# Optimization experiments

Measured on AMD Instinct MI355X. Metric: run time of the kernel, lower is better.

Reference implementation:

```python
import jax, jax.numpy as jnp
import numpy as np

N = 50000          # num nodes
E = 800000         # num edges
NUM_CLASSES = 40
FEAT_DIM = 256
FEAT_HID = 64
DEG_HID = 32
HID = 128
IN_CH = NUM_CLASSES + FEAT_HID + DEG_HID  # 136
MAX_DEG = 256      # degree-embedding table size (clip; random graph max deg << 256)


def _init_linear(key, fan_in, fan_out):
    kw, kb = jax.random.split(key)
    s = 1.0 / np.sqrt(fan_in)
    W = jax.random.uniform(kw, (fan_in, fan_out), jnp.float32, -s, s)
    b = jax.random.uniform(kb, (fan_out,), jnp.float32, -s, s)
    return W, b


def setup_inputs() -> dict:
    key = jax.random.key(0)
    ks = jax.random.split(key, 8)
    logits = jax.random.normal(ks[0], (N, NUM_CLASSES), jnp.float32)
    features = jax.random.normal(ks[1], (N, FEAT_DIM), jnp.float32)
    edge_index = jax.random.randint(ks[2], (2, E), 0, N, jnp.int32)
    Wf, bf = _init_linear(ks[3], FEAT_DIM, FEAT_HID)
    deg_table = jax.random.normal(ks[4], (MAX_DEG, DEG_HID), jnp.float32)
    W1, b1 = _init_linear(ks[5], IN_CH, HID)
    W2, b2 = _init_linear(ks[6], HID, HID)
    W3, b3 = _init_linear(ks[7], HID, NUM_CLASSES)
    return {"logits": logits, "features": features, "edge_index": edge_index,
            "Wf": Wf, "bf": bf, "deg_table": deg_table,
            "W1": W1, "b1": b1, "W2": W2, "b2": b2, "W3": W3, "b3": b3}


def reference(logits, features, edge_index, Wf, bf, deg_table, W1, b1, W2, b2, W3, b3):
    src, dst = edge_index[0], edge_index[1]
    # degree embedding: deg = degree(src) + degree(dst) on original edges
    ones_e = jnp.ones(src.shape[0], logits.dtype)
    deg = jax.ops.segment_sum(ones_e, src, num_segments=N) + \
          jax.ops.segment_sum(ones_e, dst, num_segments=N)
    deg_idx = jnp.clip(deg.astype(jnp.int32), 0, MAX_DEG - 1)
    deg_emb = deg_table[deg_idx]                              # [N, DEG_HID]

    x = jnp.concatenate([logits, features @ Wf + bf, deg_emb], axis=-1)  # [N, 136]

    # GCN normalization with self-loops (PyG gcn_norm): deg from dst column
    loop = jnp.arange(N, dtype=src.dtype)
    s = jnp.concatenate([src, loop])
    d = jnp.concatenate([dst, loop])
    dg = jax.ops.segment_sum(jnp.ones(d.shape[0], x.dtype), d, num_segments=N)
    dinv = jnp.where(dg > 0, jax.lax.rsqrt(dg), 0.0)
    norm = dinv[s] * dinv[d]                                  # [E+N]

    def conv(h, W, b):
        h = h @ W                                             # linear first
        msg = h[s] * norm[:, None]                            # gather + scale
        return jax.ops.segment_sum(msg, d, num_segments=N) + b

    x = jax.nn.relu(conv(x, W1, b1))   # dropout identity (inference)
    x = jax.nn.relu(conv(x, W2, b2))
    return conv(x, W3, b3)             # [N, NUM_CLASSES]
```

## Files before the change

kernel.cpp:

```cpp
#include <hip/hip_runtime.h>
#include <hip/hip_bf16.h>

constexpr int cN = 50000;
constexpr int cE = 800000;
constexpr int cNUM_CLASSES = 40;
constexpr int cFEAT_DIM = 256;
constexpr int cFEAT_HID = 64;
constexpr int cDEG_HID = 32;
constexpr int cHID = 128;
constexpr int cIN_CH = cNUM_CLASSES + cFEAT_HID + cDEG_HID;
constexpr int cKPAD = 160;
constexpr int cMAX_DEG = 256;
constexpr int cSCAN_NB = (cN + 255) / 256;

constexpr int cNCHUNK = 128;
constexpr int cCHUNK  = cE / cNCHUNK;
constexpr int cWORDS  = cN / 2;
constexpr int cHWORDS = cWORDS / 2;

typedef unsigned short ushort8_t __attribute__((ext_vector_type(8)));
typedef short short8_t __attribute__((ext_vector_type(8)));
typedef float float4_t __attribute__((ext_vector_type(4)));

__device__ __forceinline__ unsigned short f2bf(float f) {
    unsigned u = __builtin_bit_cast(unsigned, f);
    u += 0x7fff + ((u >> 16) & 1);
    return (unsigned short)(u >> 16);
}
__device__ __forceinline__ float bf2f(unsigned short s) {
    unsigned u = ((unsigned)s) << 16;
    return __builtin_bit_cast(float, u);
}

__global__ __launch_bounds__(256) void hist_kernel(const int* __restrict__ edge,
                                                   unsigned* __restrict__ partial) {
    __shared__ unsigned lds[cHWORDS];
    const int b = blockIdx.x, tid = threadIdx.x;
    const int cb = b & (cNCHUNK - 1);
    const int half = (b >> 7) & 1;
    const int which = b >> 8;
    for (int i = tid; i < cHWORDS; i += 256) lds[i] = 0;
    __syncthreads();
    const int* ids = edge + (size_t)which * cE + (size_t)cb * cCHUNK;
    const int lo = half * (cN / 2), hi = lo + cN / 2;
    const int wbase = half * cHWORDS;
    for (int i = tid; i < cCHUNK; i += 256) {
        int v = ids[i];
        if (v >= lo && v < hi)
            atomicAdd(&lds[(v >> 1) - wbase], 1u << ((v & 1) * 16));
    }
    __syncthreads();
    unsigned* outp = partial + ((size_t)which * cNCHUNK + cb) * cWORDS + wbase;
    for (int i = tid; i < cHWORDS; i += 256) outp[i] = lds[i];
}

__global__ __launch_bounds__(256) void merge_scan_kernel(unsigned* __restrict__ partial,
                                                         int* __restrict__ count_src,
                                                         int* __restrict__ count_dst) {
    const int w = blockIdx.x * 256 + threadIdx.x;
    if (w >= cWORDS) return;
    unsigned slo = 0, shi = 0;
    const unsigned* ps = partial + w;
    for (int c = 0; c < cNCHUNK; ++c) {
        unsigned v = ps[(size_t)c * cWORDS];
        slo += v & 0xFFFFu; shi += v >> 16;
    }
    *(int2*)&count_src[2 * w] = make_int2((int)slo, (int)shi);
    unsigned plo = 0, phi = 0;
    unsigned* pd = partial + (size_t)cNCHUNK * cWORDS + w;
    for (int c = 0; c < cNCHUNK; ++c) {
        unsigned v = pd[(size_t)c * cWORDS];
        pd[(size_t)c * cWORDS] = plo | (phi << 16);
        plo += v & 0xFFFFu; phi += v >> 16;
    }
    *(int2*)&count_dst[2 * w] = make_int2((int)plo, (int)phi);
}

__global__ __launch_bounds__(256) void block_sum_kernel(const int* __restrict__ cnt,
                                                        int* __restrict__ bsum) {
    __shared__ int s[256];
    int tid = threadIdx.x;
    int i = blockIdx.x * 256 + tid;
    int v = (i < cN) ? cnt[i] : 0;
    s[tid] = v;
    __syncthreads();
    #pragma unroll
    for (int off = 128; off > 0; off >>= 1) {
        if (tid < off) s[tid] += s[tid + off];
        __syncthreads();
    }
    if (tid == 0) bsum[blockIdx.x] = s[0];
}

__global__ __launch_bounds__(256) void scan_sums_kernel(const int* __restrict__ bsum,
                                                        int* __restrict__ boff) {
    __shared__ int s[256];
    int tid = threadIdx.x;
    int v = (tid < cSCAN_NB) ? bsum[tid] : 0;
    s[tid] = v;
    __syncthreads();
    #pragma unroll
    for (int off = 1; off < 256; off <<= 1) {
        int t = (tid >= off) ? s[tid - off] : 0;
        __syncthreads();
        s[tid] += t;
        __syncthreads();
    }
    if (tid < cSCAN_NB) boff[tid] = s[tid] - v;
}

__global__ __launch_bounds__(256) void write_rowptr_kernel(const int* __restrict__ cnt,
                                                           const int* __restrict__ boff,
                                                           int* __restrict__ rowptr,
                                                           float* __restrict__ dinv) {
    __shared__ int s[256];
    int tid = threadIdx.x;
    int i = blockIdx.x * 256 + tid;
    int v = (i < cN) ? cnt[i] : 0;
    s[tid] = v;
    __syncthreads();
    #pragma unroll
    for (int off = 1; off < 256; off <<= 1) {
        int t = (tid >= off) ? s[tid - off] : 0;
        __syncthreads();
        s[tid] += t;
        __syncthreads();
    }
    if (i < cN) {
        rowptr[i] = boff[blockIdx.x] + s[tid] - v;
        dinv[i] = rsqrtf((float)(v + 1));
    }
    if (i == 0) rowptr[cN] = cE;
}

__global__ __launch_bounds__(256) void scatter2_kernel(const int* __restrict__ edge,
                                                       const unsigned* __restrict__ partial,
                                                       const int* __restrict__ rowptr,
                                                       int* __restrict__ adj) {
    __shared__ unsigned lds[cHWORDS];
    const int b = blockIdx.x, tid = threadIdx.x;
    const int cb = b & (cNCHUNK - 1);
    const int half = b >> 7;
    const int wbase = half * cHWORDS;
    const unsigned* pp = partial + ((size_t)cNCHUNK + cb) * cWORDS + wbase;
    for (int i = tid; i < cHWORDS; i += 256) lds[i] = pp[i];
    __syncthreads();
    const int* srcs = edge + (size_t)cb * cCHUNK;
    const int* dsts = edge + cE + (size_t)cb * cCHUNK;
    const int lo = half * (cN / 2), hi = lo + cN / 2;
    for (int i = tid; i < cCHUNK; i += 256) {
        int d = dsts[i];
        if (d >= lo && d < hi) {
            int sh = (d & 1) * 16;
            unsigned old = atomicAdd(&lds[(d >> 1) - wbase], 1u << sh);
            int off = (int)((old >> sh) & 0xFFFFu);
            adj[rowptr[d] + off] = srcs[i];
        }
    }
}

__global__ __launch_bounds__(256) void wconv_kernel(const float* __restrict__ Wf,
                                                    const float* __restrict__ W1,
                                                    const float* __restrict__ W2,
                                                    const float* __restrict__ W3,
                                                    unsigned short* __restrict__ Wtf,
                                                    unsigned short* __restrict__ Wt1,
                                                    unsigned short* __restrict__ Wt2,
                                                    unsigned short* __restrict__ Wt3) {
    int i = blockIdx.x * 256 + threadIdx.x;
    if (i < 16384) {
        int n = i >> 8, k = i & 255;
        Wtf[i] = f2bf(Wf[k * cFEAT_HID + n]);
        return;
    }
    i -= 16384;
    if (i < 128 * cKPAD) {
        int n = i / cKPAD, k = i - n * cKPAD;
        Wt1[i] = (k < cIN_CH) ? f2bf(W1[k * cHID + n]) : 0;
        return;
    }
    i -= 128 * cKPAD;
    if (i < 128 * 128) {
        int n = i >> 7, k = i & 127;
        Wt2[i] = f2bf(W2[k * cHID + n]);
        return;
    }
    i -= 128 * 128;
    if (i < 48 * 128) {
        int n = i >> 7, k = i & 127;
        Wt3[i] = (n < cNUM_CLASSES) ? f2bf(W3[k * cNUM_CLASSES + n]) : 0;
    }
}

__global__ void copy_logits_kernel(const float* __restrict__ logits, unsigned short* __restrict__ xb) {
    int idx = blockIdx.x * blockDim.x + threadIdx.x;
    if (idx < cN * cNUM_CLASSES) {
        int i = idx / cNUM_CLASSES;
        int c = idx - i * cNUM_CLASSES;
        xb[(size_t)i * cKPAD + c] = f2bf(logits[idx]);
    }
}

__global__ void degemb_kernel(const int* __restrict__ count_src, const int* __restrict__ count_dst,
                              const float* __restrict__ deg_table, unsigned short* __restrict__ xb) {
    constexpr int W = cDEG_HID + 24;
    int idx = blockIdx.x * blockDim.x + threadIdx.x;
    if (idx < cN * W) {
        int i = idx / W;
        int j = idx - i * W;
        unsigned short v = 0;
        if (j < cDEG_HID) {
            int deg = count_src[i] + count_dst[i];
            if (deg > cMAX_DEG - 1) deg = cMAX_DEG - 1;
            v = f2bf(deg_table[deg * cDEG_HID + j]);
        }
        xb[(size_t)i * cKPAD + cNUM_CLASSES + cFEAT_HID + j] = v;
    }
}

template <int ASTR, int KTOT, int NT, int OSTR, int OOFF, int OUTC, bool AFP32, bool BIAS>
__global__ __launch_bounds__(256) void mfma_gemm(const void* __restrict__ Av,
                                                 const unsigned short* __restrict__ Bt,
                                                 const float* __restrict__ bias,
                                                 unsigned short* __restrict__ out) {
    __shared__ unsigned short As[64 * 32];
    __shared__ unsigned short Bs[NT * 16 * 32];

    const int tid = threadIdx.x;
    const int wave = tid >> 6;
    const int lane = tid & 63;
    const int m15 = lane & 15;
    const int q = lane >> 4;
    const int rowbase = blockIdx.x * 64;

    float4_t acc[NT];
    #pragma unroll
    for (int t = 0; t < NT; ++t) acc[t] = (float4_t){0.f, 0.f, 0.f, 0.f};

    const int arow = tid >> 2;
    const int akq = (tid & 3) * 8;
    int gr = rowbase + arow;
    if (gr > cN - 1) gr = cN - 1;

    for (int k0 = 0; k0 < KTOT; k0 += 32) {
        if constexpr (AFP32) {
            const float* ap = (const float*)Av + (size_t)gr * ASTR + k0 + akq;
            float4 v0 = *(const float4*)ap;
            float4 v1 = *(const float4*)(ap + 4);
            ushort8_t o = { f2bf(v0.x), f2bf(v0.y), f2bf(v0.z), f2bf(v0.w),
                            f2bf(v1.x), f2bf(v1.y), f2bf(v1.z), f2bf(v1.w) };
            *(ushort8_t*)&As[arow * 32 + akq] = o;
        } else {
            const unsigned short* ap = (const unsigned short*)Av + (size_t)gr * ASTR + k0 + akq;
            *(ushort8_t*)&As[arow * 32 + akq] = *(const ushort8_t*)ap;
        }
        for (int i = tid; i < NT * 64; i += 256) {
            int n = i >> 2;
            int kq = (i & 3) * 8;
            *(ushort8_t*)&Bs[n * 32 + kq] = *(const ushort8_t*)&Bt[(size_t)n * KTOT + k0 + kq];
        }
        __syncthreads();

        short8_t a = *(const short8_t*)&As[(wave * 16 + m15) * 32 + q * 8];
        #pragma unroll
        for (int t = 0; t < NT; ++t) {
            short8_t b = *(const short8_t*)&Bs[(t * 16 + m15) * 32 + q * 8];
            acc[t] = __builtin_amdgcn_mfma_f32_16x16x32_bf16(a, b, acc[t], 0, 0, 0);
        }
        __syncthreads();
    }

    #pragma unroll
    for (int t = 0; t < NT; ++t) {
        int col = t * 16 + m15;
        if (OUTC % 16 != 0 && col >= OUTC) continue;
        float bv = BIAS ? bias[col] : 0.f;
        #pragma unroll
        for (int r = 0; r < 4; ++r) {
            int row = rowbase + wave * 16 + q * 4 + r;
            if (row < cN)
                out[(size_t)row * OSTR + OOFF + col] = f2bf(acc[t][r] + bv);
        }
    }
}

template <bool RELU>
__global__ __launch_bounds__(256) void agg_bf128(const unsigned short* __restrict__ t,
                                                 const int* __restrict__ rowptr,
                                                 const int* __restrict__ adj,
                                                 const float* __restrict__ dinv,
                                                 const float* __restrict__ b,
                                                 unsigned short* __restrict__ outb) {
    const int tid = threadIdx.x;
    const int lane = tid & 15;
    const int row = blockIdx.x * 16 + (tid >> 4);
    if (row >= cN) return;
    const int c = lane * 8;
    const float di = dinv[row];
    const int beg = rowptr[row], end = rowptr[row + 1];
    float acc[8];
    #pragma unroll
    for (int k = 0; k < 8; ++k) acc[k] = 0.f;
    for (int e = beg; e < end; ++e) {
        int j = adj[e];
        float vj = dinv[j];
        ushort8_t tv = *(const ushort8_t*)&t[(size_t)j * cHID + c];
        #pragma unroll
        for (int k = 0; k < 8; ++k) acc[k] += vj * bf2f(tv[k]);
    }
    ushort8_t ts = *(const ushort8_t*)&t[(size_t)row * cHID + c];
    const float d2 = di * di;
    ushort8_t o;
    #pragma unroll
    for (int k = 0; k < 8; ++k) {
        float r = di * acc[k] + d2 * bf2f(ts[k]) + b[c + k];
        if (RELU) r = fmaxf(r, 0.f);
        o[k] = f2bf(r);
    }
    *(ushort8_t*)&outb[(size_t)row * cHID + c] = o;
}

__global__ __launch_bounds__(256) void agg_bf40(const unsigned short* __restrict__ t,
                                                const int* __restrict__ rowptr,
                                                const int* __restrict__ adj,
                                                const float* __restrict__ dinv,
                                                const float* __restrict__ b,
                                                float* __restrict__ out) {
    const int tid = threadIdx.x;
    const int lane = tid & 7;
    const int row = blockIdx.x * 32 + (tid >> 3);
    if (row >= cN) return;
    const int c = lane * 8;
    if (c >= cNUM_CLASSES) return;
    const float di = dinv[row];
    const int beg = rowptr[row], end = rowptr[row + 1];
    float acc[8];
    #pragma unroll
    for (int k = 0; k < 8; ++k) acc[k] = 0.f;
    for (int e = beg; e < end; ++e) {
        int j = adj[e];
        float vj = dinv[j];
        ushort8_t tv = *(const ushort8_t*)&t[(size_t)j * cNUM_CLASSES + c];
        #pragma unroll
        for (int k = 0; k < 8; ++k) acc[k] += vj * bf2f(tv[k]);
    }
    ushort8_t ts = *(const ushort8_t*)&t[(size_t)row * cNUM_CLASSES + c];
    const float d2 = di * di;
    float r[8];
    #pragma unroll
    for (int k = 0; k < 8; ++k) r[k] = di * acc[k] + d2 * bf2f(ts[k]) + b[c + k];
    float4 v0 = make_float4(r[0], r[1], r[2], r[3]);
    float4 v1 = make_float4(r[4], r[5], r[6], r[7]);
    *(float4*)&out[(size_t)row * cNUM_CLASSES + c] = v0;
    *(float4*)&out[(size_t)row * cNUM_CLASSES + c + 4] = v1;
}

extern "C" void kernel_launch(void* const* d_in, const int* in_sizes, int n_in,
                              void* d_out, int out_size, void* d_ws, size_t ws_size,
                              hipStream_t stream) {
    const float* logits    = (const float*)d_in[0];
    const float* features  = (const float*)d_in[1];
    const int*   edge      = (const int*)d_in[2];
    const float* Wf        = (const float*)d_in[3];
    const float* bf        = (const float*)d_in[4];
    const float* deg_table = (const float*)d_in[5];
    const float* W1        = (const float*)d_in[6];
    const float* b1        = (const float*)d_in[7];
    const float* W2        = (const float*)d_in[8];
    const float* b2        = (const float*)d_in[9];
    const float* W3        = (const float*)d_in[10];
    const float* b3        = (const float*)d_in[11];
    float* out = (float*)d_out;

    int* count_src = (int*)d_ws;
    int* count_dst = count_src + cN;
    int* rowptr    = count_dst + cN;
    int* adj       = rowptr + cN + 16;
    int* bsum      = adj + cE;
    int* boff      = bsum + 256;
    float* dinv    = (float*)(boff + 256);
    unsigned short* xb  = (unsigned short*)(dinv + cN);
    unsigned short* tb  = xb + (size_t)cN * cKPAD;
    unsigned short* hb  = tb + (size_t)cN * cHID;
    unsigned short* Wtf = hb + (size_t)cN * cHID;
    unsigned short* Wt1 = Wtf + 64 * 256;
    unsigned short* Wt2 = Wt1 + 128 * cKPAD;
    unsigned short* Wt3 = Wt2 + 128 * 128;
    unsigned* partial = (unsigned*)(Wt3 + 48 * 128);

    constexpr int WTOT = 16384 + 128 * cKPAD + 128 * 128 + 48 * 128;
    wconv_kernel<<<(WTOT + 255) / 256, 256, 0, stream>>>(Wf, W1, W2, W3, Wtf, Wt1, Wt2, Wt3);

    hist_kernel<<<512, 256, 0, stream>>>(edge, partial);
    merge_scan_kernel<<<(cWORDS + 255) / 256, 256, 0, stream>>>(partial, count_src, count_dst);
    block_sum_kernel<<<cSCAN_NB, 256, 0, stream>>>(count_dst, bsum);
    scan_sums_kernel<<<1, 256, 0, stream>>>(bsum, boff);
    write_rowptr_kernel<<<cSCAN_NB, 256, 0, stream>>>(count_dst, boff, rowptr, dinv);
    scatter2_kernel<<<256, 256, 0, stream>>>(edge, partial, rowptr, adj);

    copy_logits_kernel<<<(cN * cNUM_CLASSES + 255) / 256, 256, 0, stream>>>(logits, xb);
    degemb_kernel<<<(cN * (cDEG_HID + 24) + 255) / 256, 256, 0, stream>>>(count_src, count_dst, deg_table, xb);

    constexpr int MB = (cN + 63) / 64;

    mfma_gemm<cFEAT_DIM, 256, 4, cKPAD, cNUM_CLASSES, 64, true, true>
        <<<MB, 256, 0, stream>>>(features, Wtf, bf, xb);

    mfma_gemm<cKPAD, cKPAD, 8, cHID, 0, cHID, false, false>
        <<<MB, 256, 0, stream>>>(xb, Wt1, nullptr, tb);
    agg_bf128<true><<<(cN + 15) / 16, 256, 0, stream>>>(tb, rowptr, adj, dinv, b1, hb);

    mfma_gemm<cHID, cHID, 8, cHID, 0, cHID, false, false>
        <<<MB, 256, 0, stream>>>(hb, Wt2, nullptr, tb);
    agg_bf128<true><<<(cN + 15) / 16, 256, 0, stream>>>(tb, rowptr, adj, dinv, b2, hb);

    mfma_gemm<cHID, cHID, 3, cNUM_CLASSES, 0, cNUM_CLASSES, false, false>
        <<<MB, 256, 0, stream>>>(hb, Wt3, nullptr, tb);
    agg_bf40<<<(cN + 31) / 32, 256, 0, stream>>>(tb, rowptr, adj, dinv, b3, out);
}
```

Measured before the change: 342.5 us.

## Merge preprocessing kernels, single-pass decoupled scan, unroll and shrink aggregation blocks

Folds the weight conversion into the histogram kernel and merges logits copy with the degree-embedding fill. The three-kernel row-pointer scan becomes one kernel in which each block spins on earlier blocks' published totals. The aggregation kernels now use 128-thread blocks and take two neighbours per iteration with two accumulators, to expose more memory-level parallelism. This removes several launches and their serialization, but adds a memset and relies on all 98 scan blocks being co-resident, since blocks busy-wait on their predecessors.

```diff
diff --git a/kernel.cpp b/kernel.cpp
--- a/kernel.cpp
+++ b/kernel.cpp
@@ -11,12 +11,12 @@
 constexpr int cIN_CH = cNUM_CLASSES + cFEAT_HID + cDEG_HID;
 constexpr int cKPAD = 160;
 constexpr int cMAX_DEG = 256;
-constexpr int cSCAN_NB = (cN + 255) / 256;
 
 constexpr int cNCHUNK = 128;
 constexpr int cCHUNK  = cE / cNCHUNK;
 constexpr int cWORDS  = cN / 2;
 constexpr int cHWORDS = cWORDS / 2;
+constexpr int cSCANB  = (cWORDS + 255) / 256;
 
 typedef unsigned short ushort8_t __attribute__((ext_vector_type(8)));
 typedef short short8_t __attribute__((ext_vector_type(8)));
@@ -32,105 +32,123 @@
     return __builtin_bit_cast(float, u);
 }
 
-__global__ __launch_bounds__(256) void hist_kernel(const int* __restrict__ edge,
-                                                   unsigned* __restrict__ partial) {
+__global__ __launch_bounds__(256) void prep_kernel(const int* __restrict__ edge,
+                                                   unsigned* __restrict__ partial,
+                                                   const float* __restrict__ Wf,
+                                                   const float* __restrict__ W1,
+                                                   const float* __restrict__ W2,
+                                                   const float* __restrict__ W3,
+                                                   unsigned short* __restrict__ Wtf,
+                                                   unsigned short* __restrict__ Wt1,
+                                                   unsigned short* __restrict__ Wt2,
+                                                   unsigned short* __restrict__ Wt3) {
     __shared__ unsigned lds[cHWORDS];
     const int b = blockIdx.x, tid = threadIdx.x;
-    const int cb = b & (cNCHUNK - 1);
-    const int half = (b >> 7) & 1;
-    const int which = b >> 8;
-    for (int i = tid; i < cHWORDS; i += 256) lds[i] = 0;
+    if (b < 512) {
+        const int cb = b & (cNCHUNK - 1);
+        const int half = (b >> 7) & 1;
+        const int which = b >> 8;
+        for (int i = tid; i < cHWORDS; i += 256) lds[i] = 0;
+        __syncthreads();
+        const int* ids = edge + (size_t)which * cE + (size_t)cb * cCHUNK;
+        const int lo = half * (cN / 2), hi = lo + cN / 2;
+        const int wbase = half * cHWORDS;
+        for (int i = tid; i < cCHUNK; i += 256) {
+            int v = ids[i];
+            if (v >= lo && v < hi)
+                atomicAdd(&lds[(v >> 1) - wbase], 1u << ((v & 1) * 16));
+        }
+        __syncthreads();
+        unsigned* outp = partial + ((size_t)which * cNCHUNK + cb) * cWORDS + wbase;
+        for (int i = tid; i < cHWORDS; i += 256) outp[i] = lds[i];
+        return;
+    }
+    int i = (b - 512) * 256 + tid;
+    if (i < 16384) {
+        int n = i >> 8, k = i & 255;
+        Wtf[i] = f2bf(Wf[k * cFEAT_HID + n]);
+        return;
+    }
+    i -= 16384;
+    if (i < 128 * cKPAD) {
+        int n = i / cKPAD, k = i - n * cKPAD;
+        Wt1[i] = (k < cIN_CH) ? f2bf(W1[k * cHID + n]) : 0;
+        return;
+    }
+    i -= 128 * cKPAD;
+    if (i < 128 * 128) {
+        int n = i >> 7, k = i & 127;
+        Wt2[i] = f2bf(W2[k * cHID + n]);
+        return;
+    }
+    i -= 128 * 128;
+    if (i < 48 * 128) {
+        int n = i >> 7, k = i & 127;
+        Wt3[i] = (n < cNUM_CLASSES) ? f2bf(W3[k * cNUM_CLASSES + n]) : 0;
+    }
+}
+
+__global__ __launch_bounds__(256) void mega_scan_kernel(unsigned* __restrict__ partial,
+                                                        int* __restrict__ count_src,
+                                                        int* __restrict__ count_dst,
+                                                        int* __restrict__ rowptr,
+                                                        float* __restrict__ dinv,
+                                                        int* __restrict__ desc) {
+    const int b = blockIdx.x, tid = threadIdx.x;
+    const int w = b * 256 + tid;
+    unsigned slo = 0, shi = 0, plo = 0, phi = 0;
+    if (w < cWORDS) {
+        const unsigned* ps = partial + w;
+        for (int c = 0; c < cNCHUNK; ++c) {
+            unsigned v = ps[(size_t)c * cWORDS];
+            slo += v & 0xFFFFu; shi += v >> 16;
+        }
+        *(int2*)&count_src[2 * w] = make_int2((int)slo, (int)shi);
+        unsigned* pd = partial + (size_t)cNCHUNK * cWORDS + w;
+        for (int c = 0; c < cNCHUNK; ++c) {
+            unsigned v = pd[(size_t)c * cWORDS];
+            pd[(size_t)c * cWORDS] = plo | (phi << 16);
+            plo += v & 0xFFFFu; phi += v >> 16;
+        }
+        *(int2*)&count_dst[2 * w] = make_int2((int)plo, (int)phi);
+    }
+    __shared__ int s[256];
+    __shared__ int pre[cSCANB];
+    int tot = (int)(plo + phi);
+    s[tid] = tot;
     __syncthreads();
-    const int* ids = edge + (size_t)which * cE + (size_t)cb * cCHUNK;
-    const int lo = half * (cN / 2), hi = lo + cN / 2;
-    const int wbase = half * cHWORDS;
-    for (int i = tid; i < cCHUNK; i += 256) {
-        int v = ids[i];
-        if (v >= lo && v < hi)
-            atomicAdd(&lds[(v >> 1) - wbase], 1u << ((v & 1) * 16));
+    #pragma unroll
+    for (int off = 1; off < 256; off <<= 1) {
+        int t = (tid >= off) ? s[tid - off] : 0;
+        __syncthreads();
+        s[tid] += t;
+        __syncthreads();
+    }
+    int ex_local = s[tid] - tot;
+    int block_total = s[255];
+    if (tid == 0) atomicExch(&desc[b], block_total + 1);
+    if (tid < b) {
+        int v;
+        do { v = atomicAdd(&desc[tid], 0); } while (v == 0);
+        s[tid] = v - 1;
     }
     __syncthreads();
-    unsigned* outp = partial + ((size_t)which * cNCHUNK + cb) * cWORDS + wbase;
-    for (int i = tid; i < cHWORDS; i += 256) outp[i] = lds[i];
-}
-
-__global__ __launch_bounds__(256) void merge_scan_kernel(unsigned* __restrict__ partial,
-                                                         int* __restrict__ count_src,
-                                                         int* __restrict__ count_dst) {
-    const int w = blockIdx.x * 256 + threadIdx.x;
-    if (w >= cWORDS) return;
-    unsigned slo = 0, shi = 0;
-    const unsigned* ps = partial + w;
-    for (int c = 0; c < cNCHUNK; ++c) {
-        unsigned v = ps[(size_t)c * cWORDS];
-        slo += v & 0xFFFFu; shi += v >> 16;
-    }
-    *(int2*)&count_src[2 * w] = make_int2((int)slo, (int)shi);
-    unsigned plo = 0, phi = 0;
-    unsigned* pd = partial + (size_t)cNCHUNK * cWORDS + w;
-    for (int c = 0; c < cNCHUNK; ++c) {
-        unsigned v = pd[(size_t)c * cWORDS];
-        pd[(size_t)c * cWORDS] = plo | (phi << 16);
-        plo += v & 0xFFFFu; phi += v >> 16;
-    }
-    *(int2*)&count_dst[2 * w] = make_int2((int)plo, (int)phi);
-}
-
-__global__ __launch_bounds__(256) void block_sum_kernel(const int* __restrict__ cnt,
-                                                        int* __restrict__ bsum) {
-    __shared__ int s[256];
-    int tid = threadIdx.x;
-    int i = blockIdx.x * 256 + tid;
-    int v = (i < cN) ? cnt[i] : 0;
-    s[tid] = v;
+    if (tid >= b) s[tid] = 0;
     __syncthreads();
     #pragma unroll
     for (int off = 128; off > 0; off >>= 1) {
         if (tid < off) s[tid] += s[tid + off];
         __syncthreads();
     }
-    if (tid == 0) bsum[blockIdx.x] = s[0];
-}
-
-__global__ __launch_bounds__(256) void scan_sums_kernel(const int* __restrict__ bsum,
-                                                        int* __restrict__ boff) {
-    __shared__ int s[256];
-    int tid = threadIdx.x;
-    int v = (tid < cSCAN_NB) ? bsum[tid] : 0;
-    s[tid] = v;
-    __syncthreads();
-    #pragma unroll
-    for (int off = 1; off < 256; off <<= 1) {
-        int t = (tid >= off) ? s[tid - off] : 0;
-        __syncthreads();
-        s[tid] += t;
-        __syncthreads();
-    }
-    if (tid < cSCAN_NB) boff[tid] = s[tid] - v;
-}
-
-__global__ __launch_bounds__(256) void write_rowptr_kernel(const int* __restrict__ cnt,
-                                                           const int* __restrict__ boff,
-                                                           int* __restrict__ rowptr,
-                                                           float* __restrict__ dinv) {
-    __shared__ int s[256];
-    int tid = threadIdx.x;
-    int i = blockIdx.x * 256 + tid;
-    int v = (i < cN) ? cnt[i] : 0;
-    s[tid] = v;
-    __syncthreads();
-    #pragma unroll
-    for (int off = 1; off < 256; off <<= 1) {
-        int t = (tid >= off) ? s[tid - off] : 0;
-        __syncthreads();
-        s[tid] += t;
-        __syncthreads();
-    }
-    if (i < cN) {
-        rowptr[i] = boff[blockIdx.x] + s[tid] - v;
-        dinv[i] = rsqrtf((float)(v + 1));
-    }
-    if (i == 0) rowptr[cN] = cE;
+    int base = s[0] + ex_local;
+    if (w < cWORDS) {
+        rowptr[2 * w]     = base;
+        rowptr[2 * w + 1] = base + (int)plo;
+        dinv[2 * w]     = rsqrtf((float)(plo + 1));
+        dinv[2 * w + 1] = rsqrtf((float)(phi + 1));
+    }
+    if (b == 0 && tid == 0) rowptr[cN] = cE;
+    (void)pre;
 }
 
 __global__ __launch_bounds__(256) void scatter2_kernel(const int* __restrict__ edge,
@@ -159,62 +177,27 @@
     }
 }
 
-__global__ __launch_bounds__(256) void wconv_kernel(const float* __restrict__ Wf,
-                                                    const float* __restrict__ W1,
-                                                    const float* __restrict__ W2,
-                                                    const float* __restrict__ W3,
-                                                    unsigned short* __restrict__ Wtf,
-                                                    unsigned short* __restrict__ Wt1,
-                                                    unsigned short* __restrict__ Wt2,
-                                                    unsigned short* __restrict__ Wt3) {
-    int i = blockIdx.x * 256 + threadIdx.x;
-    if (i < 16384) {
-        int n = i >> 8, k = i & 255;
-        Wtf[i] = f2bf(Wf[k * cFEAT_HID + n]);
-        return;
-    }
-    i -= 16384;
-    if (i < 128 * cKPAD) {
-        int n = i / cKPAD, k = i - n * cKPAD;
-        Wt1[i] = (k < cIN_CH) ? f2bf(W1[k * cHID + n]) : 0;
-        return;
-    }
-    i -= 128 * cKPAD;
-    if (i < 128 * 128) {
-        int n = i >> 7, k = i & 127;
-        Wt2[i] = f2bf(W2[k * cHID + n]);
-        return;
-    }
-    i -= 128 * 128;
-    if (i < 48 * 128) {
-        int n = i >> 7, k = i & 127;
-        Wt3[i] = (n < cNUM_CLASSES) ? f2bf(W3[k * cNUM_CLASSES + n]) : 0;
-    }
-}
-
-__global__ void copy_logits_kernel(const float* __restrict__ logits, unsigned short* __restrict__ xb) {
-    int idx = blockIdx.x * blockDim.x + threadIdx.x;
-    if (idx < cN * cNUM_CLASSES) {
-        int i = idx / cNUM_CLASSES;
-        int c = idx - i * cNUM_CLASSES;
-        xb[(size_t)i * cKPAD + c] = f2bf(logits[idx]);
-    }
-}
-
-__global__ void degemb_kernel(const int* __restrict__ count_src, const int* __restrict__ count_dst,
-                              const float* __restrict__ deg_table, unsigned short* __restrict__ xb) {
-    constexpr int W = cDEG_HID + 24;
-    int idx = blockIdx.x * blockDim.x + threadIdx.x;
-    if (idx < cN * W) {
-        int i = idx / W;
-        int j = idx - i * W;
+__global__ __launch_bounds__(256) void frontend_kernel(const float* __restrict__ logits,
+                                                       const int* __restrict__ count_src,
+                                                       const int* __restrict__ count_dst,
+                                                       const float* __restrict__ deg_table,
+                                                       unsigned short* __restrict__ xb) {
+    constexpr int W = cNUM_CLASSES + cDEG_HID + 24;
+    int idx = blockIdx.x * 256 + threadIdx.x;
+    if (idx >= cN * W) return;
+    int i = idx / W;
+    int j = idx - i * W;
+    if (j < cNUM_CLASSES) {
+        xb[(size_t)i * cKPAD + j] = f2bf(logits[(size_t)i * cNUM_CLASSES + j]);
+    } else {
+        int jj = j - cNUM_CLASSES;
         unsigned short v = 0;
-        if (j < cDEG_HID) {
+        if (jj < cDEG_HID) {
             int deg = count_src[i] + count_dst[i];
             if (deg > cMAX_DEG - 1) deg = cMAX_DEG - 1;
-            v = f2bf(deg_table[deg * cDEG_HID + j]);
-        }
-        xb[(size_t)i * cKPAD + cNUM_CLASSES + cFEAT_HID + j] = v;
+            v = f2bf(deg_table[deg * cDEG_HID + jj]);
+        }
+        xb[(size_t)i * cKPAD + cNUM_CLASSES + cFEAT_HID + jj] = v;
     }
 }
 
@@ -285,7 +268,7 @@
 }
 
 template <bool RELU>
-__global__ __launch_bounds__(256) void agg_bf128(const unsigned short* __restrict__ t,
+__global__ __launch_bounds__(128) void agg_bf128(const unsigned short* __restrict__ t,
                                                  const int* __restrict__ rowptr,
                                                  const int* __restrict__ adj,
                                                  const float* __restrict__ dinv,
@@ -293,34 +276,46 @@
                                                  unsigned short* __restrict__ outb) {
     const int tid = threadIdx.x;
     const int lane = tid & 15;
-    const int row = blockIdx.x * 16 + (tid >> 4);
+    const int row = blockIdx.x * 8 + (tid >> 4);
     if (row >= cN) return;
     const int c = lane * 8;
     const float di = dinv[row];
-    const int beg = rowptr[row], end = rowptr[row + 1];
-    float acc[8];
-    #pragma unroll
-    for (int k = 0; k < 8; ++k) acc[k] = 0.f;
-    for (int e = beg; e < end; ++e) {
-        int j = adj[e];
-        float vj = dinv[j];
-        ushort8_t tv = *(const ushort8_t*)&t[(size_t)j * cHID + c];
-        #pragma unroll
-        for (int k = 0; k < 8; ++k) acc[k] += vj * bf2f(tv[k]);
+    int e = rowptr[row];
+    const int end = rowptr[row + 1];
+    float a0[8], a1[8];
+    #pragma unroll
+    for (int k = 0; k < 8; ++k) { a0[k] = 0.f; a1[k] = 0.f; }
+    for (; e + 1 < end; e += 2) {
+        int j0 = adj[e], j1 = adj[e + 1];
+        float v0 = dinv[j0], v1 = dinv[j1];
+        ushort8_t t0 = *(const ushort8_t*)&t[(size_t)j0 * cHID + c];
+        ushort8_t t1 = *(const ushort8_t*)&t[(size_t)j1 * cHID + c];
+        #pragma unroll
+        for (int k = 0; k < 8; ++k) {
+            a0[k] += v0 * bf2f(t0[k]);
+            a1[k] += v1 * bf2f(t1[k]);
+        }
+    }
+    if (e < end) {
+        int j0 = adj[e];
+        float v0 = dinv[j0];
+        ushort8_t t0 = *(const ushort8_t*)&t[(size_t)j0 * cHID + c];
+        #pragma unroll
+        for (int k = 0; k < 8; ++k) a0[k] += v0 * bf2f(t0[k]);
     }
     ushort8_t ts = *(const ushort8_t*)&t[(size_t)row * cHID + c];
     const float d2 = di * di;
     ushort8_t o;
     #pragma unroll
     for (int k = 0; k < 8; ++k) {
-        float r = di * acc[k] + d2 * bf2f(ts[k]) + b[c + k];
+        float r = di * (a0[k] + a1[k]) + d2 * bf2f(ts[k]) + b[c + k];
         if (RELU) r = fmaxf(r, 0.f);
         o[k] = f2bf(r);
     }
     *(ushort8_t*)&outb[(size_t)row * cHID + c] = o;
 }
 
-__global__ __launch_bounds__(256) void agg_bf40(const unsigned short* __restrict__ t,
+__global__ __launch_bounds__(128) void agg_bf40(const unsigned short* __restrict__ t,
                                                 const int* __restrict__ rowptr,
                                                 const int* __restrict__ adj,
                                                 const float* __restrict__ dinv,
@@ -328,27 +323,39 @@
                                                 float* __restrict__ out) {
     const int tid = threadIdx.x;
     const int lane = tid & 7;
-    const int row = blockIdx.x * 32 + (tid >> 3);
+    const int row = blockIdx.x * 16 + (tid >> 3);
     if (row >= cN) return;
     const int c = lane * 8;
     if (c >= cNUM_CLASSES) return;
     const float di = dinv[row];
-    const int beg = rowptr[row], end = rowptr[row + 1];
-    float acc[8];
-    #pragma unroll
-    for (int k = 0; k < 8; ++k) acc[k] = 0.f;
-    for (int e = beg; e < end; ++e) {
-        int j = adj[e];
-        float vj = dinv[j];
-        ushort8_t tv = *(const ushort8_t*)&t[(size_t)j * cNUM_CLASSES + c];
-        #pragma unroll
-        for (int k = 0; k < 8; ++k) acc[k] += vj * bf2f(tv[k]);
+    int e = rowptr[row];
+    const int end = rowptr[row + 1];
+    float a0[8], a1[8];
+    #pragma unroll
+    for (int k = 0; k < 8; ++k) { a0[k] = 0.f; a1[k] = 0.f; }
+    for (; e + 1 < end; e += 2) {
+        int j0 = adj[e], j1 = adj[e + 1];
+        float v0 = dinv[j0], v1 = dinv[j1];
+        ushort8_t t0 = *(const ushort8_t*)&t[(size_t)j0 * cNUM_CLASSES + c];
+        ushort8_t t1 = *(const ushort8_t*)&t[(size_t)j1 * cNUM_CLASSES + c];
+        #pragma unroll
+        for (int k = 0; k < 8; ++k) {
+            a0[k] += v0 * bf2f(t0[k]);
+            a1[k] += v1 * bf2f(t1[k]);
+        }
+    }
+    if (e < end) {
+        int j0 = adj[e];
+        float v0 = dinv[j0];
+        ushort8_t t0 = *(const ushort8_t*)&t[(size_t)j0 * cNUM_CLASSES + c];
+        #pragma unroll
+        for (int k = 0; k < 8; ++k) a0[k] += v0 * bf2f(t0[k]);
     }
     ushort8_t ts = *(const ushort8_t*)&t[(size_t)row * cNUM_CLASSES + c];
     const float d2 = di * di;
     float r[8];
     #pragma unroll
-    for (int k = 0; k < 8; ++k) r[k] = di * acc[k] + d2 * bf2f(ts[k]) + b[c + k];
+    for (int k = 0; k < 8; ++k) r[k] = di * (a0[k] + a1[k]) + d2 * bf2f(ts[k]) + b[c + k];
     float4 v0 = make_float4(r[0], r[1], r[2], r[3]);
     float4 v1 = make_float4(r[4], r[5], r[6], r[7]);
     *(float4*)&out[(size_t)row * cNUM_CLASSES + c] = v0;
@@ -376,9 +383,8 @@
     int* count_dst = count_src + cN;
     int* rowptr    = count_dst + cN;
     int* adj       = rowptr + cN + 16;
-    int* bsum      = adj + cE;
-    int* boff      = bsum + 256;
-    float* dinv    = (float*)(boff + 256);
+    int* desc      = adj + cE;
+    float* dinv    = (float*)(desc + 128);
     unsigned short* xb  = (unsigned short*)(dinv + cN);
     unsigned short* tb  = xb + (size_t)cN * cKPAD;
     unsigned short* hb  = tb + (size_t)cN * cHID;
@@ -388,18 +394,17 @@
     unsigned short* Wt3 = Wt2 + 128 * 128;
     unsigned* partial = (unsigned*)(Wt3 + 48 * 128);
 
+    hipMemsetAsync(desc, 0, 128 * sizeof(int), stream);
+
     constexpr int WTOT = 16384 + 128 * cKPAD + 128 * 128 + 48 * 128;
-    wconv_kernel<<<(WTOT + 255) / 256, 256, 0, stream>>>(Wf, W1, W2, W3, Wtf, Wt1, Wt2, Wt3);
-
-    hist_kernel<<<512, 256, 0, stream>>>(edge, partial);
-    merge_scan_kernel<<<(cWORDS + 255) / 256, 256, 0, stream>>>(partial, count_src, count_dst);
-    block_sum_kernel<<<cSCAN_NB, 256, 0, stream>>>(count_dst, bsum);
-    scan_sums_kernel<<<1, 256, 0, stream>>>(bsum, boff);
-    write_rowptr_kernel<<<cSCAN_NB, 256, 0, stream>>>(count_dst, boff, rowptr, dinv);
+    constexpr int WBLK = (WTOT + 255) / 256;
+    prep_kernel<<<512 + WBLK, 256, 0, stream>>>(edge, partial, Wf, W1, W2, W3, Wtf, Wt1, Wt2, Wt3);
+
+    mega_scan_kernel<<<cSCANB, 256, 0, stream>>>(partial, count_src, count_dst, rowptr, dinv, desc);
+
     scatter2_kernel<<<256, 256, 0, stream>>>(edge, partial, rowptr, adj);
 
-    copy_logits_kernel<<<(cN * cNUM_CLASSES + 255) / 256, 256, 0, stream>>>(logits, xb);
-    degemb_kernel<<<(cN * (cDEG_HID + 24) + 255) / 256, 256, 0, stream>>>(count_src, count_dst, deg_table, xb);
+    frontend_kernel<<<(cN * 96 + 255) / 256, 256, 0, stream>>>(logits, count_src, count_dst, deg_table, xb);
 
     constexpr int MB = (cN + 63) / 64;
 
@@ -408,13 +413,13 @@
 
     mfma_gemm<cKPAD, cKPAD, 8, cHID, 0, cHID, false, false>
         <<<MB, 256, 0, stream>>>(xb, Wt1, nullptr, tb);
-    agg_bf128<true><<<(cN + 15) / 16, 256, 0, stream>>>(tb, rowptr, adj, dinv, b1, hb);
+    agg_bf128<true><<<(cN + 7) / 8, 128, 0, stream>>>(tb, rowptr, adj, dinv, b1, hb);
 
     mfma_gemm<cHID, cHID, 8, cHID, 0, cHID, false, false>
         <<<MB, 256, 0, stream>>>(hb, Wt2, nullptr, tb);
-    agg_bf128<true><<<(cN + 15) / 16, 256, 0, stream>>>(tb, rowptr, adj, dinv, b2, hb);
+    agg_bf128<true><<<(cN + 7) / 8, 128, 0, stream>>>(tb, rowptr, adj, dinv, b2, hb);
 
     mfma_gemm<cHID, cHID, 3, cNUM_CLASSES, 0, cNUM_CLASSES, false, false>
         <<<MB, 256, 0, stream>>>(hb, Wt3, nullptr, tb);
-    agg_bf40<<<(cN + 31) / 32, 256, 0, stream>>>(tb, rowptr, adj, dinv, b3, out);
-}
+    agg_bf40<<<(cN + 15) / 16, 128, 0, stream>>>(tb, rowptr, adj, dinv, b3, out);
+}
```

New measurement: 322.9 us. -5.7%, faster.
